# Performance work log

Measured on AMD Instinct MI355X. Metric: run time of the kernel, lower is better.

The kernel has to match this reference:

```python
import jax, jax.numpy as jnp
import numpy as np

N_VARS, N_CONS, N_EDGES = 200000, 100000, 1200000
VF, CF, H, R = 7, 5, 64, 2

def _glorot(k, shape):
    lim = 1.0 / np.sqrt(shape[-1])
    return jax.random.uniform(k, shape, jnp.float32, -lim, lim)

def setup_inputs() -> dict:
    key = jax.random.key(0)
    ks = jax.random.split(key, 20)
    return {
        "var_features": jax.random.normal(ks[0], (N_VARS, VF), jnp.float32),
        "con_features": jax.random.normal(ks[1], (N_CONS, CF), jnp.float32),
        "edge_var": jax.random.randint(ks[2], (N_EDGES,), 0, N_VARS, jnp.int32),
        "edge_con": jax.random.randint(ks[3], (N_EDGES,), 0, N_CONS, jnp.int32),
        # var encoder MLP (depth=1): in->hidden (tanh), hidden->out
        "W_ve1": _glorot(ks[4], (H, VF)), "b_ve1": jnp.zeros((H,), jnp.float32),
        "W_ve2": _glorot(ks[5], (H, H)),  "b_ve2": jnp.zeros((H,), jnp.float32),
        # con encoder MLP
        "W_ce1": _glorot(ks[6], (H, CF)), "b_ce1": jnp.zeros((H,), jnp.float32),
        "W_ce2": _glorot(ks[7], (H, H)),  "b_ce2": jnp.zeros((H,), jnp.float32),
        # per-round message linears, stacked over rounds
        "W_v2c": _glorot(ks[8], (R, H, H)), "b_v2c": jnp.zeros((R, H), jnp.float32),
        "W_c2v": _glorot(ks[9], (R, H, H)), "b_c2v": jnp.zeros((R, H), jnp.float32),
        # readout
        "W_ro": _glorot(ks[10], (1, H)), "b_ro": jnp.zeros((1,), jnp.float32),
    }

def reference(var_features, con_features, edge_var, edge_con,
              W_ve1, b_ve1, W_ve2, b_ve2,
              W_ce1, b_ce1, W_ce2, b_ce2,
              W_v2c, b_v2c, W_c2v, b_c2v,
              W_ro, b_ro):
    n_vars = var_features.shape[0]
    n_cons = con_features.shape[0]
    # encoders: eqx.nn.MLP(depth=1) = Linear -> tanh -> Linear
    h_var = jnp.tanh(var_features @ W_ve1.T + b_ve1) @ W_ve2.T + b_ve2  # (n_vars, H)
    h_con = jnp.tanh(con_features @ W_ce1.T + b_ce1) @ W_ce2.T + b_ce2  # (n_cons, H)
    n_rounds = W_v2c.shape[0]
    for r in range(n_rounds):
        # var -> con: gather, linear, scatter-add, tanh
        msg_v = h_var[edge_var] @ W_v2c[r].T + b_v2c[r]                 # (n_edges, H)
        agg_c = jax.ops.segment_sum(msg_v, edge_con, num_segments=n_cons)
        h_con = jnp.tanh(h_con + agg_c)
        # con -> var
        msg_c = h_con[edge_con] @ W_c2v[r].T + b_c2v[r]                 # (n_edges, H)
        agg_v = jax.ops.segment_sum(msg_c, edge_var, num_segments=n_vars)
        h_var = jnp.tanh(h_var + agg_v)
    scores = (h_var @ W_ro.T + b_ro).squeeze(-1)                        # (n_vars,)
    return scores
```

## Files before the change

kernel.cpp:

```cpp
#include <hip/hip_runtime.h>
#include <hip/hip_bf16.h>
#include <hip/hip_fp16.h>

#define WPB 4
#define SCAN_EPB 1024

#define CSB 384
#define BSH 7
#define BWID 128

typedef _Float16 h8 __attribute__((ext_vector_type(8)));
typedef float f32x4 __attribute__((ext_vector_type(4)));

__device__ __forceinline__ float bcast(float v, int i) {
  return __builtin_bit_cast(float, __builtin_amdgcn_readlane(__builtin_bit_cast(int, v), i));
}
__device__ __forceinline__ h8 h8zero() {
  h8 r;
#pragma unroll
  for (int j = 0; j < 8; ++j) r[j] = (_Float16)0;
  return r;
}
__device__ __forceinline__ h8 cvt8(float4 a, float4 b) {
  h8 r;
  r[0] = (_Float16)a.x; r[1] = (_Float16)a.y; r[2] = (_Float16)a.z; r[3] = (_Float16)a.w;
  r[4] = (_Float16)b.x; r[5] = (_Float16)b.y; r[6] = (_Float16)b.z; r[7] = (_Float16)b.w;
  return r;
}

template<int IN_F>
__global__ __launch_bounds__(256, 4) void encoder_mfma_kernel(
    const float* __restrict__ x,
    const float* __restrict__ W1, const float* __restrict__ b1,
    const h8* __restrict__ W2h, const float* __restrict__ b2,
    __half* __restrict__ out, int n_rows) {
  __shared__ _Float16 hlds[WPB][16][64];
  int t = threadIdx.x;
  int wave = t >> 6, lane = t & 63;
  int mm = lane & 15, fb = lane >> 4;

  float w1reg[IN_F];
#pragma unroll
  for (int j = 0; j < IN_F; ++j) w1reg[j] = W1[lane * IN_F + j];
  float b1v = b1[lane];

  h8 Bf[4][2];
  float bvt[4];
#pragma unroll
  for (int tt = 0; tt < 4; ++tt) {
#pragma unroll
    for (int s = 0; s < 2; ++s) Bf[tt][s] = W2h[(tt * 2 + s) * 64 + lane];
    bvt[tt] = b2[16 * tt + mm];
  }

  int c0 = ((fb ^ (mm & 7)) << 3);
  int c1 = (((4 + fb) ^ (mm & 7)) << 3);

  const int ntot = n_rows * IN_F;
  int stride16 = gridDim.x * WPB * 16;
  for (int rowb = (blockIdx.x * WPB + wave) * 16; rowb < n_rows; rowb += stride16) {
    int base = rowb * IN_F;
    float xa = 0.0f, xb = 0.0f;
    if (base + lane < ntot) xa = x[base + lane];
    if (base + 64 + lane < ntot) xb = x[base + 64 + lane];

#pragma unroll
    for (int r = 0; r < 16; ++r) {
      float h = b1v;
#pragma unroll
      for (int j = 0; j < IN_F; ++j) {
        int idx = r * IN_F + j;
        float xv;
        if (idx < 64) xv = bcast(xa, idx); else xv = bcast(xb, idx - 64);
        h += w1reg[j] * xv;
      }
      int sc = ((((lane >> 3) ^ (r & 7)) << 3) | (lane & 7));
      hlds[wave][r][sc] = (_Float16)tanhf(h);
    }

    h8 a0 = *(const h8*)&hlds[wave][mm][c0];
    h8 a1 = *(const h8*)&hlds[wave][mm][c1];

    f32x4 d[4];
#pragma unroll
    for (int tt = 0; tt < 4; ++tt) {
      f32x4 dz; dz[0] = bvt[tt]; dz[1] = bvt[tt]; dz[2] = bvt[tt]; dz[3] = bvt[tt];
      d[tt] = __builtin_amdgcn_mfma_f32_16x16x32_f16(a0, Bf[tt][0], dz, 0, 0, 0);
      d[tt] = __builtin_amdgcn_mfma_f32_16x16x32_f16(a1, Bf[tt][1], d[tt], 0, 0, 0);
    }

#pragma unroll
    for (int i = 0; i < 4; ++i) {
      int grow = rowb + fb * 4 + i;
      if (grow < n_rows) {
#pragma unroll
        for (int tt = 0; tt < 4; ++tt)
          out[(size_t)grow * 64 + 16 * tt + mm] = __float2half(d[tt][i]);
      }
    }
  }
}


__global__ __launch_bounds__(256) void bucket_hist_kernel(
    const int* __restrict__ ev, const int* __restrict__ ec,
    int* __restrict__ partial, int n_edges, int n_vars, int nbuckets) {
  extern __shared__ int cnt[];
  int t = threadIdx.x;
  for (int i = t; i < nbuckets; i += 256) cnt[i] = 0;
  __syncthreads();
  int chunk = (n_edges + CSB - 1) / CSB;
  int lo = blockIdx.x * chunk;
  int hi = lo + chunk; if (hi > n_edges) hi = n_edges;
  for (int e = lo + t; e < hi; e += 256) {
    int v = ev[e], c = ec[e];
    atomicAdd(&cnt[v >> BSH], 1);
    atomicAdd(&cnt[(n_vars + c) >> BSH], 1);
  }
  __syncthreads();
  for (int i = t; i < nbuckets; i += 256)
    partial[(size_t)i * CSB + blockIdx.x] = cnt[i];
}

__global__ __launch_bounds__(256) void bucket_place_kernel(
    const int* __restrict__ ev, const int* __restrict__ ec,
    const int* __restrict__ scanned, unsigned int* __restrict__ keypay,
    int n_edges, int n_vars, int nbuckets) {
  extern __shared__ int cur[];
  int t = threadIdx.x;
  for (int i = t; i < nbuckets; i += 256)
    cur[i] = scanned[(size_t)i * CSB + blockIdx.x];
  __syncthreads();
  int chunk = (n_edges + CSB - 1) / CSB;
  int lo = blockIdx.x * chunk;
  int hi = lo + chunk; if (hi > n_edges) hi = n_edges;
  for (int e = lo + t; e < hi; e += 256) {
    int v = ev[e], c = ec[e];
    int mc = n_vars + c;
    int s1 = atomicAdd(&cur[v >> BSH], 1);
    keypay[s1] = ((unsigned)(v & (BWID - 1)) << 25) | (unsigned)c;
    int s2 = atomicAdd(&cur[mc >> BSH], 1);
    keypay[s2] = ((unsigned)(mc & (BWID - 1)) << 25) | (unsigned)v;
  }
}

__global__ __launch_bounds__(256) void csr_fine_kernel(
    const unsigned int* __restrict__ keypay, const int* __restrict__ scanned,
    int* __restrict__ rp, int* __restrict__ esrc,
    int n_nodes, int nbuckets, int total) {
  __shared__ int cnt[BWID];
  __shared__ int pfx[BWID];
  __shared__ int cur[BWID];
  int j = blockIdx.x;
  int t = threadIdx.x;
  int bstart = scanned[(size_t)j * CSB];
  int bend   = scanned[(size_t)(j + 1) * CSB];
  if (t < BWID) cnt[t] = 0;
  __syncthreads();
  for (int i = bstart + t; i < bend; i += 256)
    atomicAdd(&cnt[keypay[i] >> 25], 1);
  __syncthreads();
  if (t < BWID) pfx[t] = cnt[t];
  __syncthreads();
  for (int off = 1; off < BWID; off <<= 1) {
    int add = (t < BWID && t >= off) ? pfx[t - off] : 0;
    __syncthreads();
    if (t < BWID) pfx[t] += add;
    __syncthreads();
  }
  if (t < BWID) {
    int ex = pfx[t] - cnt[t];
    cur[t] = ex;
    int node = j * BWID + t;
    if (node < n_nodes) rp[node] = bstart + ex;
  }
  if (j == 0 && t == 0) rp[n_nodes] = total;
  __syncthreads();
  for (int i = bstart + t; i < bend; i += 256) {
    unsigned int kp = keypay[i];
    int off = atomicAdd(&cur[kp >> 25], 1);
    esrc[bstart + off] = (int)(kp & 0x1FFFFFFu);
  }
}

__global__ __launch_bounds__(256) void wcvt_kernel(
    const float* __restrict__ W, h8* __restrict__ Wh, int total) {
  int tid = blockIdx.x * 256 + threadIdx.x;
  if (tid >= total) return;
  int l = tid & 63;
  int f = (tid >> 6) & 7;
  int r = tid >> 9;
  int tt = f >> 1, s = f & 1;
  const float* wp = W + (size_t)r * 4096 + (size_t)(16 * tt + (l & 15)) * 64
                    + 32 * s + 8 * (l >> 4);
  Wh[tid] = cvt8(*(const float4*)wp, *(const float4*)(wp + 4));
}

__global__ __launch_bounds__(256) void scan_blocks_kernel(
    const int* __restrict__ in, int* __restrict__ out,
    int* __restrict__ bsums, int n) {
  __shared__ int s[256];
  int t = threadIdx.x;
  int base = blockIdx.x * SCAN_EPB + t * 4;
  int v[4]; int local = 0;
#pragma unroll
  for (int j = 0; j < 4; ++j) {
    int idx = base + j;
    v[j] = (idx < n) ? in[idx] : 0;
    local += v[j];
  }
  s[t] = local;
  __syncthreads();
  for (int off = 1; off < 256; off <<= 1) {
    int val = (t >= off) ? s[t - off] : 0;
    __syncthreads();
    s[t] += val;
    __syncthreads();
  }
  int run = s[t] - local;
#pragma unroll
  for (int j = 0; j < 4; ++j) {
    int idx = base + j;
    if (idx < n) out[idx] = run;
    run += v[j];
  }
  if (t == 255) bsums[blockIdx.x] = s[255];
}

__global__ __launch_bounds__(256) void scan_sums_kernel(int* __restrict__ bsums, int nb) {
  __shared__ int s[256];
  int t = threadIdx.x;
  int base = t * 4;
  int v[4]; int local = 0;
#pragma unroll
  for (int j = 0; j < 4; ++j) {
    int idx = base + j;
    v[j] = (idx < nb) ? bsums[idx] : 0;
    local += v[j];
  }
  s[t] = local;
  __syncthreads();
  for (int off = 1; off < 256; off <<= 1) {
    int val = (t >= off) ? s[t - off] : 0;
    __syncthreads();
    s[t] += val;
    __syncthreads();
  }
  int run = s[t] - local;
#pragma unroll
  for (int j = 0; j < 4; ++j) {
    int idx = base + j;
    if (idx < nb) bsums[idx] = run;
    run += v[j];
  }
}

__global__ __launch_bounds__(256) void scan_add_kernel(
    int* __restrict__ out, const int* __restrict__ bsums, int n, int total) {
  int t = threadIdx.x;
  int base = blockIdx.x * SCAN_EPB + t * 4;
  int add = bsums[blockIdx.x];
#pragma unroll
  for (int j = 0; j < 4; ++j) {
    int idx = base + j;
    if (idx < n) out[idx] += add;
  }
  if (blockIdx.x == 0 && t == 0) out[n] = total;
}

template<bool RO>
__global__ __launch_bounds__(256, 8) void fused_mfma_kernel(
    __half* __restrict__ hdst, const __half* __restrict__ hsrc,
    const int* __restrict__ rp, const int* __restrict__ esrc,
    const h8* __restrict__ Wh, const float* __restrict__ b,
    const float* __restrict__ Wro, const float* __restrict__ bro,
    float* __restrict__ scores, int n_rows, int zrow) {
  int t = threadIdx.x;
  int wave = t >> 6, lane = t & 63;
  int mm = lane & 15;
  int fb = lane >> 4;

  float brov = RO ? bro[0] : 0.0f;

  const float4* rows4 = (const float4*)hsrc;

  int stride16 = gridDim.x * WPB * 16;
  for (int rowb = (blockIdx.x * WPB + wave) * 16; rowb < n_rows; rowb += stride16) {
    int mrow = rowb + mm;
    int mc = (mrow < n_rows) ? mrow : n_rows - 1;
    int p = rp[mc], end = rp[mc + 1];
    float degf = (float)(end - p);

    h8 a0 = h8zero(), a1 = h8zero();
    while (__any(p < end)) {
      bool v0 = p < end, v1 = p + 1 < end;
      int i0 = v0 ? p : 0;
      int i1 = v1 ? p + 1 : 0;
      int s0 = esrc[i0];
      int s1 = esrc[i1];
      s0 = v0 ? s0 : zrow;
      s1 = v1 ? s1 : zrow;
      float4 q0a = rows4[(size_t)s0 * 8 + fb];
      float4 q0b = rows4[(size_t)s0 * 8 + 4 + fb];
      float4 q1a = rows4[(size_t)s1 * 8 + fb];
      float4 q1b = rows4[(size_t)s1 * 8 + 4 + fb];
      a0 += __builtin_bit_cast(h8, q0a);
      a1 += __builtin_bit_cast(h8, q0b);
      a0 += __builtin_bit_cast(h8, q1a);
      a1 += __builtin_bit_cast(h8, q1b);
      p += 2;
    }

    int zoff = 0;
    asm volatile("" : "+v"(zoff));
    const h8* Whb = Wh + zoff;
    const float* bb = b + zoff;
    const float* wrob = RO ? (Wro + zoff) : nullptr;

    float pr[4] = {0.f, 0.f, 0.f, 0.f};
#pragma unroll
    for (int h = 0; h < 2; ++h) {
      __builtin_amdgcn_sched_barrier(0);
      h8 Bf[2][2];
      float bvt[2], wrot[2];
#pragma unroll
      for (int s = 0; s < 2; ++s) {
        int tt = 2 * h + s;
#pragma unroll
        for (int ks = 0; ks < 2; ++ks)
          Bf[s][ks] = Whb[(tt * 2 + ks) * 64 + lane];
        bvt[s] = bb[16 * tt + mm];
        wrot[s] = RO ? wrob[16 * tt + mm] : 0.0f;
      }

      f32x4 d[2];
#pragma unroll
      for (int s = 0; s < 2; ++s) {
        f32x4 dz; dz[0] = 0.f; dz[1] = 0.f; dz[2] = 0.f; dz[3] = 0.f;
        d[s] = __builtin_amdgcn_mfma_f32_16x16x32_f16(a0, Bf[s][0], dz, 0, 0, 0);
        d[s] = __builtin_amdgcn_mfma_f32_16x16x32_f16(a1, Bf[s][1], d[s], 0, 0, 0);
      }

#pragma unroll
      for (int i = 0; i < 4; ++i) {
        float deg_i = __shfl(degf, fb * 4 + i, 64);
        int grow = rowb + fb * 4 + i;
        bool ok = grow < n_rows;
#pragma unroll
        for (int s = 0; s < 2; ++s) {
          int tt = 2 * h + s;
          size_t addr = (size_t)grow * 64 + 16 * tt + mm;
          float hold = ok ? __half2float(hdst[addr]) : 0.0f;
          float hv = tanhf(hold + bvt[s] * deg_i + d[s][i]);
          if (RO) {
            pr[i] += hv * wrot[s];
          } else {
            if (ok) hdst[addr] = __float2half(hv);
          }
        }
      }
    }

    if (RO) {
#pragma unroll
      for (int i = 0; i < 4; ++i) {
        float pv = pr[i];
        pv += __shfl_xor(pv, 1, 64);
        pv += __shfl_xor(pv, 2, 64);
        pv += __shfl_xor(pv, 4, 64);
        pv += __shfl_xor(pv, 8, 64);
        int grow = rowb + fb * 4 + i;
        if (mm == 0 && grow < n_rows) scores[grow] = pv + brov;
      }
    }
  }
}

static inline int rowgrid16(int n) {
  int want = (n + WPB * 16 - 1) / (WPB * 16);
  return want < 2048 ? want : 2048;
}

extern "C" void kernel_launch(void* const* d_in, const int* in_sizes, int n_in,
                              void* d_out, int out_size, void* d_ws, size_t ws_size,
                              hipStream_t stream) {
  const float* vf    = (const float*)d_in[0];
  const float* cf    = (const float*)d_in[1];
  const int*   ev    = (const int*)d_in[2];
  const int*   ec    = (const int*)d_in[3];
  const float* W_ve1 = (const float*)d_in[4];
  const float* b_ve1 = (const float*)d_in[5];
  const float* W_ve2 = (const float*)d_in[6];
  const float* b_ve2 = (const float*)d_in[7];
  const float* W_ce1 = (const float*)d_in[8];
  const float* b_ce1 = (const float*)d_in[9];
  const float* W_ce2 = (const float*)d_in[10];
  const float* b_ce2 = (const float*)d_in[11];
  const float* W_v2c = (const float*)d_in[12];
  const float* b_v2c = (const float*)d_in[13];
  const float* W_c2v = (const float*)d_in[14];
  const float* b_c2v = (const float*)d_in[15];
  const float* W_ro  = (const float*)d_in[16];
  const float* b_ro  = (const float*)d_in[17];

  const int n_vars  = in_sizes[0] / 7;
  const int n_cons  = in_sizes[1] / 5;
  const int n_edges = in_sizes[2];
  const int R       = in_sizes[12] / (64 * 64);
  const int n_nodes = n_vars + n_cons;

  char* p = (char*)d_ws;
  __half* h_var = (__half*)p; p += ((size_t)n_vars + 1) * 64 * 2;
  __half* h_con = (__half*)p; p += ((size_t)n_cons + 1) * 64 * 2;
  int*   rp     = (int*)p;   p += (size_t)(n_nodes + 1) * 4;
  int*   esrc   = (int*)p;   p += (size_t)2 * n_edges * 4;
  int*   bsums  = (int*)p;   p += 1024 * 4;
  h8*    wh_v2c = (h8*)p;    p += (size_t)R * 512 * 16;
  h8*    wh_c2v = (h8*)p;    p += (size_t)R * 512 * 16;
  h8*    wh_ve2 = (h8*)p;    p += (size_t)512 * 16;
  h8*    wh_ce2 = (h8*)p;    p += (size_t)512 * 16;

  const int nbuckets = (n_nodes + BWID - 1) >> BSH;
  const int nP = nbuckets * CSB;
  int* partial = (int*)h_var;
  int* scanned = partial + (size_t)(nP + 1);
  unsigned int* keypay = (unsigned int*)h_con;

  const int nb2 = (nP + SCAN_EPB - 1) / SCAN_EPB;

  bucket_hist_kernel<<<CSB, 256, nbuckets * 4, stream>>>(
      ev, ec, partial, n_edges, n_vars, nbuckets);

  wcvt_kernel<<<(R * 512 + 255) / 256, 256, 0, stream>>>(W_v2c, wh_v2c, R * 512);
  wcvt_kernel<<<(R * 512 + 255) / 256, 256, 0, stream>>>(W_c2v, wh_c2v, R * 512);
  wcvt_kernel<<<2, 256, 0, stream>>>(W_ve2, wh_ve2, 512);
  wcvt_kernel<<<2, 256, 0, stream>>>(W_ce2, wh_ce2, 512);

  scan_blocks_kernel<<<nb2, 256, 0, stream>>>(partial, scanned, bsums, nP);
  scan_sums_kernel<<<1, 256, 0, stream>>>(bsums, nb2);
  scan_add_kernel<<<nb2, 256, 0, stream>>>(scanned, bsums, nP, 2 * n_edges);

  bucket_place_kernel<<<CSB, 256, nbuckets * 4, stream>>>(
      ev, ec, scanned, keypay, n_edges, n_vars, nbuckets);
  csr_fine_kernel<<<nbuckets, 256, 0, stream>>>(
      keypay, scanned, rp, esrc, n_nodes, nbuckets, 2 * n_edges);

  hipMemsetAsync(h_var + (size_t)n_vars * 64, 0, 128, stream);
  hipMemsetAsync(h_con + (size_t)n_cons * 64, 0, 128, stream);

  encoder_mfma_kernel<7><<<rowgrid16(n_vars), 256, 0, stream>>>(
      vf, W_ve1, b_ve1, wh_ve2, b_ve2, h_var, n_vars);
  encoder_mfma_kernel<5><<<rowgrid16(n_cons), 256, 0, stream>>>(
      cf, W_ce1, b_ce1, wh_ce2, b_ce2, h_con, n_cons);

  for (int r = 0; r < R; ++r) {
    fused_mfma_kernel<false><<<rowgrid16(n_cons), 256, 0, stream>>>(
        h_con, h_var, rp + n_vars, esrc,
        wh_v2c + (size_t)r * 512, b_v2c + (size_t)r * 64,
        nullptr, nullptr, nullptr, n_cons, n_vars);
    if (r == R - 1) {
      fused_mfma_kernel<true><<<rowgrid16(n_vars), 256, 0, stream>>>(
          h_var, h_con, rp, esrc,
          wh_c2v + (size_t)r * 512, b_c2v + (size_t)r * 64,
          W_ro, b_ro, (float*)d_out, n_vars, n_cons);
    } else {
      fused_mfma_kernel<false><<<rowgrid16(n_vars), 256, 0, stream>>>(
          h_var, h_con, rp, esrc,
          wh_c2v + (size_t)r * 512, b_c2v + (size_t)r * 64,
          nullptr, nullptr, nullptr, n_vars, n_cons);
    }
  }
}
```

Measured before the change: 391.0 us.

## Software-pipeline CSR gather loop with double-buffered four-edge row prefetch

The neighbour gather loop now handles four edges per step instead of two and runs as a double-buffered pipeline. Indices for the next group and row data for the group after it are loaded while the current group is accumulated, so more memory requests are in flight per wave. To give the compiler room for the extra live registers, the launch bounds drop from 8 to 5 waves per SIMD, which lowers occupancy. Rows with low degree may also fetch more padding work per row.

```diff
diff --git a/kernel.cpp b/kernel.cpp
--- a/kernel.cpp
+++ b/kernel.cpp
@@ -269,7 +269,7 @@
 }
 
 template<bool RO>
-__global__ __launch_bounds__(256, 8) void fused_mfma_kernel(
+__global__ __launch_bounds__(256, 5) void fused_mfma_kernel(
     __half* __restrict__ hdst, const __half* __restrict__ hsrc,
     const int* __restrict__ rp, const int* __restrict__ esrc,
     const h8* __restrict__ Wh, const float* __restrict__ b,
@@ -292,23 +292,65 @@
     float degf = (float)(end - p);
 
     h8 a0 = h8zero(), a1 = h8zero();
+
+    int s0, s1, s2, s3, t0, t1, t2, t3;
+    {
+      bool w0 = p < end, w1 = p + 1 < end, w2 = p + 2 < end, w3 = p + 3 < end;
+      int x0 = esrc[w0 ? p : 0], x1 = esrc[w1 ? p + 1 : 0];
+      int x2 = esrc[w2 ? p + 2 : 0], x3 = esrc[w3 ? p + 3 : 0];
+      s0 = w0 ? x0 : zrow; s1 = w1 ? x1 : zrow;
+      s2 = w2 ? x2 : zrow; s3 = w3 ? x3 : zrow;
+    }
+    float4 A0a = rows4[(size_t)s0 * 8 + fb], A0b = rows4[(size_t)s0 * 8 + 4 + fb];
+    float4 A1a = rows4[(size_t)s1 * 8 + fb], A1b = rows4[(size_t)s1 * 8 + 4 + fb];
+    float4 A2a = rows4[(size_t)s2 * 8 + fb], A2b = rows4[(size_t)s2 * 8 + 4 + fb];
+    float4 A3a = rows4[(size_t)s3 * 8 + fb], A3b = rows4[(size_t)s3 * 8 + 4 + fb];
+    {
+      int q = p + 4;
+      bool w0 = q < end, w1 = q + 1 < end, w2 = q + 2 < end, w3 = q + 3 < end;
+      int x0 = esrc[w0 ? q : 0], x1 = esrc[w1 ? q + 1 : 0];
+      int x2 = esrc[w2 ? q + 2 : 0], x3 = esrc[w3 ? q + 3 : 0];
+      t0 = w0 ? x0 : zrow; t1 = w1 ? x1 : zrow;
+      t2 = w2 ? x2 : zrow; t3 = w3 ? x3 : zrow;
+    }
+
     while (__any(p < end)) {
-      bool v0 = p < end, v1 = p + 1 < end;
-      int i0 = v0 ? p : 0;
-      int i1 = v1 ? p + 1 : 0;
-      int s0 = esrc[i0];
-      int s1 = esrc[i1];
-      s0 = v0 ? s0 : zrow;
-      s1 = v1 ? s1 : zrow;
-      float4 q0a = rows4[(size_t)s0 * 8 + fb];
-      float4 q0b = rows4[(size_t)s0 * 8 + 4 + fb];
-      float4 q1a = rows4[(size_t)s1 * 8 + fb];
-      float4 q1b = rows4[(size_t)s1 * 8 + 4 + fb];
-      a0 += __builtin_bit_cast(h8, q0a);
-      a1 += __builtin_bit_cast(h8, q0b);
-      a0 += __builtin_bit_cast(h8, q1a);
-      a1 += __builtin_bit_cast(h8, q1b);
-      p += 2;
+      float4 B0a = rows4[(size_t)t0 * 8 + fb], B0b = rows4[(size_t)t0 * 8 + 4 + fb];
+      float4 B1a = rows4[(size_t)t1 * 8 + fb], B1b = rows4[(size_t)t1 * 8 + 4 + fb];
+      float4 B2a = rows4[(size_t)t2 * 8 + fb], B2b = rows4[(size_t)t2 * 8 + 4 + fb];
+      float4 B3a = rows4[(size_t)t3 * 8 + fb], B3b = rows4[(size_t)t3 * 8 + 4 + fb];
+      {
+        int q = p + 8;
+        bool w0 = q < end, w1 = q + 1 < end, w2 = q + 2 < end, w3 = q + 3 < end;
+        int x0 = esrc[w0 ? q : 0], x1 = esrc[w1 ? q + 1 : 0];
+        int x2 = esrc[w2 ? q + 2 : 0], x3 = esrc[w3 ? q + 3 : 0];
+        s0 = w0 ? x0 : zrow; s1 = w1 ? x1 : zrow;
+        s2 = w2 ? x2 : zrow; s3 = w3 ? x3 : zrow;
+      }
+      a0 += __builtin_bit_cast(h8, A0a); a1 += __builtin_bit_cast(h8, A0b);
+      a0 += __builtin_bit_cast(h8, A1a); a1 += __builtin_bit_cast(h8, A1b);
+      a0 += __builtin_bit_cast(h8, A2a); a1 += __builtin_bit_cast(h8, A2b);
+      a0 += __builtin_bit_cast(h8, A3a); a1 += __builtin_bit_cast(h8, A3b);
+      p += 4;
+      if (!__any(p < end)) break;
+
+      A0a = rows4[(size_t)s0 * 8 + fb]; A0b = rows4[(size_t)s0 * 8 + 4 + fb];
+      A1a = rows4[(size_t)s1 * 8 + fb]; A1b = rows4[(size_t)s1 * 8 + 4 + fb];
+      A2a = rows4[(size_t)s2 * 8 + fb]; A2b = rows4[(size_t)s2 * 8 + 4 + fb];
+      A3a = rows4[(size_t)s3 * 8 + fb]; A3b = rows4[(size_t)s3 * 8 + 4 + fb];
+      {
+        int q = p + 8;
+        bool w0 = q < end, w1 = q + 1 < end, w2 = q + 2 < end, w3 = q + 3 < end;
+        int x0 = esrc[w0 ? q : 0], x1 = esrc[w1 ? q + 1 : 0];
+        int x2 = esrc[w2 ? q + 2 : 0], x3 = esrc[w3 ? q + 3 : 0];
+        t0 = w0 ? x0 : zrow; t1 = w1 ? x1 : zrow;
+        t2 = w2 ? x2 : zrow; t3 = w3 ? x3 : zrow;
+      }
+      a0 += __builtin_bit_cast(h8, B0a); a1 += __builtin_bit_cast(h8, B0b);
+      a0 += __builtin_bit_cast(h8, B1a); a1 += __builtin_bit_cast(h8, B1b);
+      a0 += __builtin_bit_cast(h8, B2a); a1 += __builtin_bit_cast(h8, B2b);
+      a0 += __builtin_bit_cast(h8, B3a); a1 += __builtin_bit_cast(h8, B3b);
+      p += 4;
     }
 
     int zoff = 0;
```

After: 386.6 us. Within noise of the previous version (-1.1%).
